# Kernel optimization log

Measured on AMD Instinct MI355X. Metric: run time of the kernel, lower is better.

The kernel has to match this reference:

```python
import jax, jax.numpy as jnp
import numpy as np

ENTITY_SIZE = 100000
RELATION_SIZE = 500
DIM = 128
BATCH = 8192
MARGIN = 1.0


def _xavier_normal(key, shape):
    fan_in, fan_out = shape[1], shape[0]
    std = float(np.sqrt(2.0 / (fan_in + fan_out)))
    return jax.random.normal(key, shape, dtype=jnp.float32) * std


def setup_inputs() -> dict:
    key = jax.random.key(0)
    k1, k2, k3, k4, k5 = jax.random.split(key, 5)
    entities = _xavier_normal(k1, (ENTITY_SIZE, DIM))
    relations = _xavier_normal(k2, (RELATION_SIZE, DIM))
    transfer_matrix = _xavier_normal(k3, (RELATION_SIZE, DIM * DIM))
    positive_triples = jax.random.randint(k4, (BATCH, 3), 0, RELATION_SIZE, dtype=jnp.int32).astype(jnp.int64)
    negative_triples = jax.random.randint(k5, (BATCH, 3), 0, RELATION_SIZE, dtype=jnp.int32).astype(jnp.int64)
    return {
        "positive_triples": positive_triples,
        "negative_triples": negative_triples,
        "entities": entities,
        "relations": relations,
        "transfer_matrix": transfer_matrix,
    }


def _l2_normalize(x, eps=1e-12):
    # matches F.normalize(x, 2, -1): x / max(||x||_2, eps)
    n = jnp.linalg.norm(x, ord=2, axis=-1, keepdims=True)
    return x / jnp.maximum(n, eps)


def _calc_score(triples, entities, relations, transfer_matrix):
    heads, rels, tails = triples[:, 0], triples[:, 1], triples[:, 2]
    h = entities[heads]                      # [B, D]
    r = relations[rels]                      # [B, D]
    t = entities[tails]                      # [B, D]
    Mr = transfer_matrix[rels].reshape(-1, DIM, DIM)  # [B, D, D]
    # per-relation transfer: row-vector times matrix
    h = jnp.einsum('bd,bde->be', h, Mr)
    t = jnp.einsum('bd,bde->be', t, Mr)
    h = _l2_normalize(h)
    r = _l2_normalize(r)
    t = _l2_normalize(t)
    return jnp.sum(jnp.abs(h + r - t), axis=-1)  # L1 norm per triple, [B]


def reference(positive_triples, negative_triples, entities, relations, transfer_matrix):
    pos = _calc_score(positive_triples, entities, relations, transfer_matrix)
    neg = _calc_score(negative_triples, entities, relations, transfer_matrix)
    # MarginRankingLoss(margin=1.0) with target = -1:
    # mean(max(0, -y*(pos - neg) + margin)) = mean(relu(pos - neg + margin))
    return jnp.mean(jax.nn.relu(pos - neg + MARGIN))
```

## Files before the change

kernel.cpp:

```cpp
#include <hip/hip_runtime.h>
#include <math.h>

#define DIM 128
#define BATCH 8192
#define NTRIP (2 * BATCH)
#define NREL 500
#define MARGIN 1.0f
#define CAP 96
#define BSTR 136

typedef __attribute__((ext_vector_type(8))) short short8;
typedef __attribute__((ext_vector_type(4))) short short4v;
typedef __attribute__((ext_vector_type(4))) float f32x4;

__device__ __forceinline__ float wave_sum(float v) {
    v += __shfl_xor(v, 32, 64);
    v += __shfl_xor(v, 16, 64);
    v += __shfl_xor(v, 8, 64);
    v += __shfl_xor(v, 4, 64);
    v += __shfl_xor(v, 2, 64);
    v += __shfl_xor(v, 1, 64);
    return v;
}

__device__ __forceinline__ float quad_sum(float v) {
    v += __shfl_xor(v, 1, 64);
    v += __shfl_xor(v, 2, 64);
    v += __shfl_xor(v, 4, 64);
    v += __shfl_xor(v, 8, 64);
    return v;
}

__device__ __forceinline__ short f2bf(float f) {
    unsigned u = __float_as_uint(f);
    u = (u + 0x7fffu + ((u >> 16) & 1u)) >> 16;
    return (short)u;
}

__global__ __launch_bounds__(256)
void transr_bucket(const int* __restrict__ pos, const int* __restrict__ neg,
                   int* __restrict__ rel_count, int2* __restrict__ ht,
                   int* __restrict__ ids) {
    const int gid = blockIdx.x * 256 + threadIdx.x;
    const int* trip = (gid < BATCH) ? (pos + gid * 3) : (neg + (gid - BATCH) * 3);
    const int h = trip[0], r = trip[1], t = trip[2];
    const int slot = atomicAdd(&rel_count[r], 1);
    if (slot < CAP) {
        ht[r * CAP + slot] = make_int2(h, t);
        ids[r * CAP + slot] = gid;
    }
}

__global__ __launch_bounds__(512)
void transr_main(const float* __restrict__ entities,
                 const float* __restrict__ relations,
                 const float* __restrict__ transfer,
                 const int* __restrict__ rel_count,
                 const int2* __restrict__ ht, const int* __restrict__ ids,
                 float* __restrict__ scores, int* __restrict__ done,
                 float* __restrict__ out) {
    __shared__ __align__(16) short Bt[DIM * BSTR];
    __shared__ float rhat_s[DIM];
    __shared__ float lred[8];
    __shared__ int lflag;

    const int rel = blockIdx.x;
    const int tid = threadIdx.x;
    const int cnt = min(rel_count[rel], CAP);

    const int lane = tid & 63;
    const int w = tid >> 6;
    const int n = lane & 15;
    const int q = lane >> 4;
    const int jm = n >> 1;
    const int sel = n & 1;

    if (tid < DIM) rhat_s[tid] = relations[(size_t)rel * DIM + tid];

    const int2* __restrict__ ht_rel = ht + rel * CAP;
    const int* __restrict__ ids_rel = ids + rel * CAP;
    const int ntiles = (cnt + 7) >> 3;
    int2 pair0 = make_int2(0, 0);
    if (w < ntiles && cnt > 0) pair0 = ht_rel[min(w * 8 + jm, cnt - 1)];

    const float4* __restrict__ mrf4 = (const float4*)(transfer + (size_t)rel * (DIM * DIM));
    const int m = tid & 31;
    const int g = tid >> 5;
    const int n0 = m * 4;
#pragma unroll
    for (int it = 0; it < 2; ++it) {
        const int f0 = it * 2048 + g * 128 + m;
        const float4 v0 = mrf4[f0];
        const float4 v1 = mrf4[f0 + 32];
        const float4 v2 = mrf4[f0 + 64];
        const float4 v3 = mrf4[f0 + 96];
        const int k0 = it * 64 + g * 4;
        const float* p0 = (const float*)&v0;
        const float* p1 = (const float*)&v1;
        const float* p2 = (const float*)&v2;
        const float* p3 = (const float*)&v3;
#pragma unroll
        for (int j = 0; j < 4; ++j) {
            short4v wv;
            wv[0] = f2bf(p0[j]);
            wv[1] = f2bf(p1[j]);
            wv[2] = f2bf(p2[j]);
            wv[3] = f2bf(p3[j]);
            *(short4v*)(&Bt[(n0 + j) * BSTR + k0]) = wv;
        }
    }
    __syncthreads();
    if (tid < 64) {
        const float a = rhat_s[tid], b = rhat_s[tid + 64];
        const float ss = wave_sum(fmaf(a, a, b * b));
        if (tid == 0) lred[0] = 1.0f / fmaxf(sqrtf(ss), 1e-12f);
    }
    __syncthreads();
    const float rinv = lred[0];

    float r_reg[8];
#pragma unroll
    for (int nt = 0; nt < 8; ++nt) r_reg[nt] = rhat_s[nt * 16 + n] * rinv;

    for (int tile = w; tile < ntiles; tile += 8) {
        const int2 pair = (tile == w) ? pair0 : ht_rel[min(tile * 8 + jm, cnt - 1)];
        const float* __restrict__ erow = entities + (size_t)(sel ? pair.y : pair.x) * DIM;

        short8 af[4];
#pragma unroll
        for (int kc = 0; kc < 4; ++kc) {
            const float4 u0 = *(const float4*)(erow + kc * 32 + q * 8);
            const float4 u1 = *(const float4*)(erow + kc * 32 + q * 8 + 4);
            short8 a;
            a[0] = f2bf(u0.x); a[1] = f2bf(u0.y); a[2] = f2bf(u0.z); a[3] = f2bf(u0.w);
            a[4] = f2bf(u1.x); a[5] = f2bf(u1.y); a[6] = f2bf(u1.z); a[7] = f2bf(u1.w);
            af[kc] = a;
        }

        f32x4 acc[8];
#pragma unroll
        for (int nt = 0; nt < 8; ++nt) acc[nt] = (f32x4){0.0f, 0.0f, 0.0f, 0.0f};
#pragma unroll
        for (int nt = 0; nt < 8; ++nt) {
            const short* __restrict__ bp = &Bt[(nt * 16 + n) * BSTR + q * 8];
#pragma unroll
            for (int kc = 0; kc < 4; ++kc) {
                const short8 bfr = *(const short8*)(bp + kc * 32);
                acc[nt] = __builtin_amdgcn_mfma_f32_16x16x32_bf16(af[kc], bfr, acc[nt], 0, 0, 0);
            }
        }

#pragma unroll
        for (int p = 0; p < 4; p += 2) {
            float hs = 0.0f, ts = 0.0f;
#pragma unroll
            for (int nt = 0; nt < 8; ++nt) {
                hs = fmaf(acc[nt][p], acc[nt][p], hs);
                ts = fmaf(acc[nt][p + 1], acc[nt][p + 1], ts);
            }
            hs = quad_sum(hs);
            ts = quad_sum(ts);
            const float invh = 1.0f / fmaxf(sqrtf(hs), 1e-12f);
            const float invt = 1.0f / fmaxf(sqrtf(ts), 1e-12f);
            float ss = 0.0f;
#pragma unroll
            for (int nt = 0; nt < 8; ++nt)
                ss += fabsf(fmaf(acc[nt][p], invh, r_reg[nt]) - acc[nt][p + 1] * invt);
            ss = quad_sum(ss);
            if (n == 0) {
                const int jS = min(tile * 8 + (q * 2 + (p >> 1)), cnt - 1);
                __hip_atomic_store(&scores[ids_rel[jS]], ss,
                                   __ATOMIC_RELAXED, __HIP_MEMORY_SCOPE_AGENT);
            }
        }
    }

    __syncthreads();
    if (tid == 0) {
        __threadfence();
        const int old = atomicAdd(done, 1);
        lflag = (old == NREL - 1) ? 1 : 0;
    }
    __syncthreads();
    if (lflag) {
        __threadfence();
        float ss = 0.0f;
        for (int i = tid; i < BATCH; i += 512) {
            const float a = __hip_atomic_load(&scores[i], __ATOMIC_RELAXED, __HIP_MEMORY_SCOPE_AGENT);
            const float b = __hip_atomic_load(&scores[BATCH + i], __ATOMIC_RELAXED, __HIP_MEMORY_SCOPE_AGENT);
            const float d = a - b + MARGIN;
            ss += (d > 0.0f) ? d : 0.0f;
        }
        ss = wave_sum(ss);
        if (lane == 0) lred[w] = ss;
        __syncthreads();
        if (tid == 0) {
            float t = 0.0f;
#pragma unroll
            for (int i = 0; i < 8; ++i) t += lred[i];
            out[0] = t * (1.0f / (float)BATCH);
        }
    }
}

extern "C" void kernel_launch(void* const* d_in, const int* in_sizes, int n_in,
                              void* d_out, int out_size, void* d_ws, size_t ws_size,
                              hipStream_t stream) {
    const int*   pos       = (const int*)d_in[0];
    const int*   neg       = (const int*)d_in[1];
    const float* entities  = (const float*)d_in[2];
    const float* relations = (const float*)d_in[3];
    const float* transfer  = (const float*)d_in[4];
    float* out = (float*)d_out;

    int*   wsi       = (int*)d_ws;
    float* scores    = (float*)d_ws;
    int*   rel_count = wsi + 16384;
    int*   done      = wsi + 16884;
    int*   ids       = wsi + 16896;
    int2*  ht        = (int2*)(wsi + 65536);

    hipMemsetAsync(rel_count, 0, 501 * sizeof(int), stream);
    transr_bucket<<<NTRIP / 256, 256, 0, stream>>>(pos, neg, rel_count, ht, ids);
    transr_main<<<NREL, 512, 0, stream>>>(entities, relations, transfer, rel_count,
                                          ht, ids, scores, done, out);
}
```

Baseline: 131.4 us.

## Fuse relation bucketing into main kernel via per-block scan of all triples

Drops the separate bucketing kernel and its global-atomic histogram. Each of the 500 blocks now scans all 16384 triples and collects the ones matching its relation into shared memory with shared atomics. This removes one launch and the global ht/ids round-trip, at the cost of every block reading the full triple arrays (about 200KB each, mostly served from L2). The memset now only resets the done counter.

Result: slower. 136.0 us (+3.5%).

```diff
diff --git a/kernel.cpp b/kernel.cpp
--- a/kernel.cpp
+++ b/kernel.cpp
@@ -37,37 +37,23 @@
     return (short)u;
 }
 
-__global__ __launch_bounds__(256)
-void transr_bucket(const int* __restrict__ pos, const int* __restrict__ neg,
-                   int* __restrict__ rel_count, int2* __restrict__ ht,
-                   int* __restrict__ ids) {
-    const int gid = blockIdx.x * 256 + threadIdx.x;
-    const int* trip = (gid < BATCH) ? (pos + gid * 3) : (neg + (gid - BATCH) * 3);
-    const int h = trip[0], r = trip[1], t = trip[2];
-    const int slot = atomicAdd(&rel_count[r], 1);
-    if (slot < CAP) {
-        ht[r * CAP + slot] = make_int2(h, t);
-        ids[r * CAP + slot] = gid;
-    }
-}
-
 __global__ __launch_bounds__(512)
-void transr_main(const float* __restrict__ entities,
+void transr_main(const int* __restrict__ pos, const int* __restrict__ neg,
+                 const float* __restrict__ entities,
                  const float* __restrict__ relations,
                  const float* __restrict__ transfer,
-                 const int* __restrict__ rel_count,
-                 const int2* __restrict__ ht, const int* __restrict__ ids,
                  float* __restrict__ scores, int* __restrict__ done,
                  float* __restrict__ out) {
     __shared__ __align__(16) short Bt[DIM * BSTR];
     __shared__ float rhat_s[DIM];
+    __shared__ int2 htL[CAP];
+    __shared__ int idsL[CAP];
+    __shared__ int cntL;
     __shared__ float lred[8];
     __shared__ int lflag;
 
     const int rel = blockIdx.x;
     const int tid = threadIdx.x;
-    const int cnt = min(rel_count[rel], CAP);
-
     const int lane = tid & 63;
     const int w = tid >> 6;
     const int n = lane & 15;
@@ -76,12 +62,19 @@
     const int sel = n & 1;
 
     if (tid < DIM) rhat_s[tid] = relations[(size_t)rel * DIM + tid];
-
-    const int2* __restrict__ ht_rel = ht + rel * CAP;
-    const int* __restrict__ ids_rel = ids + rel * CAP;
-    const int ntiles = (cnt + 7) >> 3;
-    int2 pair0 = make_int2(0, 0);
-    if (w < ntiles && cnt > 0) pair0 = ht_rel[min(w * 8 + jm, cnt - 1)];
+    if (tid == 0) cntL = 0;
+    __syncthreads();
+
+    for (int i = tid; i < NTRIP; i += 512) {
+        const int* trip = (i < BATCH) ? (pos + i * 3) : (neg + (i - BATCH) * 3);
+        if (trip[1] == rel) {
+            const int slot = atomicAdd(&cntL, 1);
+            if (slot < CAP) {
+                htL[slot] = make_int2(trip[0], trip[2]);
+                idsL[slot] = i;
+            }
+        }
+    }
 
     const float4* __restrict__ mrf4 = (const float4*)(transfer + (size_t)rel * (DIM * DIM));
     const int m = tid & 31;
@@ -110,67 +103,70 @@
         }
     }
     __syncthreads();
-    if (tid < 64) {
-        const float a = rhat_s[tid], b = rhat_s[tid + 64];
+
+    const int cnt = min(cntL, CAP);
+    const int ntiles = (cnt + 7) >> 3;
+
+    {
+        const float a = rhat_s[lane], b = rhat_s[lane + 64];
         const float ss = wave_sum(fmaf(a, a, b * b));
-        if (tid == 0) lred[0] = 1.0f / fmaxf(sqrtf(ss), 1e-12f);
-    }
-    __syncthreads();
-    const float rinv = lred[0];
-
-    float r_reg[8];
-#pragma unroll
-    for (int nt = 0; nt < 8; ++nt) r_reg[nt] = rhat_s[nt * 16 + n] * rinv;
-
-    for (int tile = w; tile < ntiles; tile += 8) {
-        const int2 pair = (tile == w) ? pair0 : ht_rel[min(tile * 8 + jm, cnt - 1)];
-        const float* __restrict__ erow = entities + (size_t)(sel ? pair.y : pair.x) * DIM;
-
-        short8 af[4];
-#pragma unroll
-        for (int kc = 0; kc < 4; ++kc) {
-            const float4 u0 = *(const float4*)(erow + kc * 32 + q * 8);
-            const float4 u1 = *(const float4*)(erow + kc * 32 + q * 8 + 4);
-            short8 a;
-            a[0] = f2bf(u0.x); a[1] = f2bf(u0.y); a[2] = f2bf(u0.z); a[3] = f2bf(u0.w);
-            a[4] = f2bf(u1.x); a[5] = f2bf(u1.y); a[6] = f2bf(u1.z); a[7] = f2bf(u1.w);
-            af[kc] = a;
-        }
-
-        f32x4 acc[8];
-#pragma unroll
-        for (int nt = 0; nt < 8; ++nt) acc[nt] = (f32x4){0.0f, 0.0f, 0.0f, 0.0f};
-#pragma unroll
-        for (int nt = 0; nt < 8; ++nt) {
-            const short* __restrict__ bp = &Bt[(nt * 16 + n) * BSTR + q * 8];
+        const float rinv = 1.0f / fmaxf(sqrtf(ss), 1e-12f);
+
+        float r_reg[8];
+#pragma unroll
+        for (int nt = 0; nt < 8; ++nt) r_reg[nt] = rhat_s[nt * 16 + n] * rinv;
+
+        for (int tile = w; tile < ntiles; tile += 8) {
+            const int jA = min(tile * 8 + jm, cnt - 1);
+            const int2 pair = htL[jA];
+            const float* __restrict__ erow = entities + (size_t)(sel ? pair.y : pair.x) * DIM;
+
+            short8 af[4];
 #pragma unroll
             for (int kc = 0; kc < 4; ++kc) {
-                const short8 bfr = *(const short8*)(bp + kc * 32);
-                acc[nt] = __builtin_amdgcn_mfma_f32_16x16x32_bf16(af[kc], bfr, acc[nt], 0, 0, 0);
-            }
-        }
-
-#pragma unroll
-        for (int p = 0; p < 4; p += 2) {
-            float hs = 0.0f, ts = 0.0f;
+                const float4 u0 = *(const float4*)(erow + kc * 32 + q * 8);
+                const float4 u1 = *(const float4*)(erow + kc * 32 + q * 8 + 4);
+                short8 a;
+                a[0] = f2bf(u0.x); a[1] = f2bf(u0.y); a[2] = f2bf(u0.z); a[3] = f2bf(u0.w);
+                a[4] = f2bf(u1.x); a[5] = f2bf(u1.y); a[6] = f2bf(u1.z); a[7] = f2bf(u1.w);
+                af[kc] = a;
+            }
+
+            f32x4 acc[8];
+#pragma unroll
+            for (int nt = 0; nt < 8; ++nt) acc[nt] = (f32x4){0.0f, 0.0f, 0.0f, 0.0f};
 #pragma unroll
             for (int nt = 0; nt < 8; ++nt) {
-                hs = fmaf(acc[nt][p], acc[nt][p], hs);
-                ts = fmaf(acc[nt][p + 1], acc[nt][p + 1], ts);
-            }
-            hs = quad_sum(hs);
-            ts = quad_sum(ts);
-            const float invh = 1.0f / fmaxf(sqrtf(hs), 1e-12f);
-            const float invt = 1.0f / fmaxf(sqrtf(ts), 1e-12f);
-            float ss = 0.0f;
-#pragma unroll
-            for (int nt = 0; nt < 8; ++nt)
-                ss += fabsf(fmaf(acc[nt][p], invh, r_reg[nt]) - acc[nt][p + 1] * invt);
-            ss = quad_sum(ss);
-            if (n == 0) {
-                const int jS = min(tile * 8 + (q * 2 + (p >> 1)), cnt - 1);
-                __hip_atomic_store(&scores[ids_rel[jS]], ss,
-                                   __ATOMIC_RELAXED, __HIP_MEMORY_SCOPE_AGENT);
+                const short* __restrict__ bp = &Bt[(nt * 16 + n) * BSTR + q * 8];
+#pragma unroll
+                for (int kc = 0; kc < 4; ++kc) {
+                    const short8 bfr = *(const short8*)(bp + kc * 32);
+                    acc[nt] = __builtin_amdgcn_mfma_f32_16x16x32_bf16(af[kc], bfr, acc[nt], 0, 0, 0);
+                }
+            }
+
+#pragma unroll
+            for (int p = 0; p < 4; p += 2) {
+                float hs = 0.0f, ts = 0.0f;
+#pragma unroll
+                for (int nt = 0; nt < 8; ++nt) {
+                    hs = fmaf(acc[nt][p], acc[nt][p], hs);
+                    ts = fmaf(acc[nt][p + 1], acc[nt][p + 1], ts);
+                }
+                hs = quad_sum(hs);
+                ts = quad_sum(ts);
+                const float invh = 1.0f / fmaxf(sqrtf(hs), 1e-12f);
+                const float invt = 1.0f / fmaxf(sqrtf(ts), 1e-12f);
+                float ss2 = 0.0f;
+#pragma unroll
+                for (int nt = 0; nt < 8; ++nt)
+                    ss2 += fabsf(fmaf(acc[nt][p], invh, r_reg[nt]) - acc[nt][p + 1] * invt);
+                ss2 = quad_sum(ss2);
+                if (n == 0) {
+                    const int jS = min(tile * 8 + (q * 2 + (p >> 1)), cnt - 1);
+                    __hip_atomic_store(&scores[idsL[jS]], ss2,
+                                       __ATOMIC_RELAXED, __HIP_MEMORY_SCOPE_AGENT);
+                }
             }
         }
     }
@@ -213,15 +209,11 @@
     const float* transfer  = (const float*)d_in[4];
     float* out = (float*)d_out;
 
-    int*   wsi       = (int*)d_ws;
-    float* scores    = (float*)d_ws;
-    int*   rel_count = wsi + 16384;
-    int*   done      = wsi + 16884;
-    int*   ids       = wsi + 16896;
-    int2*  ht        = (int2*)(wsi + 65536);
-
-    hipMemsetAsync(rel_count, 0, 501 * sizeof(int), stream);
-    transr_bucket<<<NTRIP / 256, 256, 0, stream>>>(pos, neg, rel_count, ht, ids);
-    transr_main<<<NREL, 512, 0, stream>>>(entities, relations, transfer, rel_count,
-                                          ht, ids, scores, done, out);
-}
+    int*   wsi    = (int*)d_ws;
+    float* scores = (float*)d_ws;
+    int*   done   = wsi + 16384;
+
+    hipMemsetAsync(done, 0, sizeof(int), stream);
+    transr_main<<<NREL, 512, 0, stream>>>(pos, neg, entities, relations, transfer,
+                                          scores, done, out);
+}
```
